# Performance work log

Measured on AMD Instinct MI355X. Metric: run time of the kernel, lower is better.

The kernel has to match this reference:

```python
import jax, jax.numpy as jnp
import numpy as np

KERNEL = 5
DILATIONS = (3, 1)
N_HEADS = 8
LN_EPS = 1e-5


def unfold1d(x, kernel, dilation, pad):
    # x: (N, H, S) -> (N, H, S, kernel) dilated sliding windows (same length)
    xp = jnp.pad(x, ((0, 0), (0, 0), (pad, pad)))
    S = x.shape[-1]
    idx = jnp.arange(S)[:, None] + jnp.arange(kernel)[None, :] * dilation  # (S, K)
    return xp[:, :, idx]  # (N, H, S, K)


def dilated_mha(q, k, v, Ws, bs, Wo, bo):
    # q,k,v: (B, S, D); Ws: (2, split, split); Wo: (D, D)
    B, S, D = q.shape
    ndil = len(DILATIONS)
    hpd = N_HEADS // ndil            # heads per dilation
    dk = D // N_HEADS
    split = D // ndil
    scale = dk ** (-0.5)
    outs, probs = [], []
    for i, dil in enumerate(DILATIONS):
        pad = dil * (KERNEL - 1) // 2
        sl = slice(i * split, (i + 1) * split)
        qi = q[..., sl] @ Ws[i].T + bs[i]
        ki = k[..., sl] @ Ws[i].T + bs[i]
        vi = v[..., sl] @ Ws[i].T + bs[i]
        # (B,S,hpd,dk) -> (B,dk,hpd,S), matching torch transpose(1,2).permute(0,3,1,2)
        to4 = lambda x: jnp.transpose(x.reshape(B, S, hpd, dk), (0, 3, 2, 1))
        qi4, ki4, vi4 = to4(qi), to4(ki), to4(vi)
        # unfold then reinterpret (B*dk,hpd,...) as (B*hpd,dk,...) exactly as torch .reshape does
        kp = unfold1d(ki4.reshape(B * dk, hpd, S), KERNEL, dil, pad).reshape(B * hpd, dk, S, KERNEL)
        vp = unfold1d(vi4.reshape(B * dk, hpd, S), KERNEL, dil, pad).reshape(B * hpd, dk, S, KERNEL)
        qr = qi4.reshape(B * hpd, dk, S)
        scores = jnp.einsum('nds,ndsk->nsk', qr, kp) * scale   # (B*hpd, S, K)
        p = jax.nn.softmax(scores, axis=-1)
        out = jnp.einsum('nsk,ndsk->nds', p, vp)               # (B*hpd, dk, S)
        out = jnp.transpose(out.reshape(B, hpd, dk, S), (0, 3, 1, 2)).reshape(B, S, split)
        outs.append(out)
        probs.append(p.reshape(B, hpd, S, KERNEL))
    o = jnp.concatenate(outs, axis=-1) @ Wo.T + bo
    return o, jnp.concatenate(probs, axis=1)


def layer_norm(x, g, b):
    mu = jnp.mean(x, axis=-1, keepdims=True)
    var = jnp.mean((x - mu) ** 2, axis=-1, keepdims=True)
    return (x - mu) * jax.lax.rsqrt(var + LN_EPS) * g + b


def setup_inputs() -> dict:
    key = jax.random.key(0)
    ks = jax.random.split(key, 6)
    B, S, D = 32, 2048, 256
    split = D // 2
    q_emb = jax.random.normal(ks[0], (B, S, D), dtype=jnp.float32)
    s_emb = jax.random.normal(ks[1], (B, S, D), dtype=jnp.float32)
    lens = jax.random.randint(ks[2], (B,), 5, S, dtype=jnp.int32)
    W_lin = jax.random.normal(ks[3], (3, 2, split, split), dtype=jnp.float32) * (split ** -0.5)
    b_lin = jnp.zeros((3, 2, split), dtype=jnp.float32)
    W_out = jax.random.normal(ks[4], (3, D, D), dtype=jnp.float32) * (D ** -0.5)
    b_out = jnp.zeros((3, D), dtype=jnp.float32)
    ln_g = jnp.ones((3, D), dtype=jnp.float32)
    ln_b = jnp.zeros((3, D), dtype=jnp.float32)
    return {"q_emb": q_emb, "s_emb": s_emb, "lens": lens, "W_lin": W_lin,
            "b_lin": b_lin, "W_out": W_out, "b_out": b_out, "ln_g": ln_g, "ln_b": ln_b}


def reference(q_emb, s_emb, lens, W_lin, b_lin, W_out, b_out, ln_g, ln_b):
    # CASTransformer.forward, shortcut=True path, eval mode (dropout=id, mask unused)
    a1, _ = dilated_mha(q_emb, q_emb, q_emb, W_lin[0], b_lin[0], W_out[0], b_out[0])
    hq = layer_norm(q_emb + a1, ln_g[0], ln_b[0])
    a2, q_scores = dilated_mha(s_emb, s_emb, s_emb, W_lin[1], b_lin[1], W_out[1], b_out[1])
    hs = layer_norm(s_emb + a2, ln_g[1], ln_b[1])
    a3, _ = dilated_mha(hq, hq, hs, W_lin[2], b_lin[2], W_out[2], b_out[2])
    z = layer_norm(hq + a3, ln_g[2], ln_b[2])
    return z, q_scores
```

## Files before the change

kernel.cpp:

```cpp
#include <hip/hip_runtime.h>
#include <hip/hip_bf16.h>

typedef __bf16 bf16x8 __attribute__((ext_vector_type(8)));
typedef float  f32x4  __attribute__((ext_vector_type(4)));
typedef unsigned int u32;
typedef u32 u32x4 __attribute__((ext_vector_type(4)));
typedef unsigned short ushort_t;

__device__ inline float bf2f(ushort_t h) {
    union { u32 u; float f; } v; v.u = ((u32)h) << 16; return v.f;
}
__device__ inline ushort_t f2bf(float f) {
    union { float f; u32 u; } v; v.f = f;
    u32 u = v.u;
    return (ushort_t)((u + 0x7fffu + ((u >> 16) & 1u)) >> 16);
}
__device__ inline bf16x8 load_bf8(const ushort_t* p) {
    u32x4 u = *reinterpret_cast<const u32x4*>(p);
    return __builtin_bit_cast(bf16x8, u);
}
__device__ inline bf16x8 load8_in(const void* base, size_t idx, int f32flag) {
    if (!f32flag) return load_bf8((const ushort_t*)base + idx);
    const float* pf = (const float*)base + idx;
    f32x4 a = *reinterpret_cast<const f32x4*>(pf);
    f32x4 b = *reinterpret_cast<const f32x4*>(pf + 4);
    bf16x8 r;
#pragma unroll
    for (int j = 0; j < 4; ++j) { r[j] = (__bf16)a[j]; r[4 + j] = (__bf16)b[j]; }
    return r;
}
__device__ inline float ld_in(const void* base, size_t idx, int f32flag) {
    return f32flag ? ((const float*)base)[idx] : bf2f(((const ushort_t*)base)[idx]);
}

__device__ inline int pofs(int row, int ch) { return row * 256 + (ch ^ ((row & 15) << 3)); }
__device__ inline int tofs(int tr, int ch) { return tr * 256 + (ch ^ (((tr + 8) & 15) << 3)); }

__device__ inline int f_of(const int* flags, int i) { return i < 0 ? 0 : flags[i]; }
__device__ inline int out_f32(const int* flags) {
    return flags[0] | flags[1] | flags[3] | flags[4] | flags[5] | flags[6] | flags[7] | flags[8];
}

__global__ __launch_bounds__(256) void detect_all(
    const u32* a0, const u32* a1, const u32* a2, const u32* a3,
    const u32* a4, const u32* a5, const u32* a6, const u32* a7,
    int* __restrict__ flags)
{
    const u32* arrs[8] = {a0, a1, a2, a3, a4, a5, a6, a7};
    const int  ns[8]   = {16384, 16384, 16384, 384, 16384, 384, 384, 384};
    const int  fi[8]   = {0, 1, 3, 4, 5, 6, 7, 8};
    const int  b = blockIdx.x;
    const u32* d = arrs[b];
    const int  n = ns[b];

    const int t = threadIdx.x;
    int cn = 0, co = 0;
    for (int i = t; i < n; i += 256) {
        const u32 w = d[i];
        const u32 e  = (w >> 7) & 0xFF;
        const u32 fe = (w >> 23) & 0xFF;
        cn += (e >= 100 && e <= 135) ? 1 : 0;
        co += (((w & 0xFFFFu) == 0u) && fe >= 100 && fe <= 140) ? 1 : 0;
    }
    __shared__ int sn[256], so[256];
    sn[t] = cn; so[t] = co; __syncthreads();
    for (int o = 128; o; o >>= 1) {
        if (t < o) { sn[t] += sn[t + o]; so[t] += so[t + o]; }
        __syncthreads();
    }
    if (t == 0) {
        const int CN = sn[0], CO = so[0];
        const int is_f32 = (2 * CN < n) && ((2 * CO > n) || (20 * CN > n));
        flags[fi[b]] = is_f32 ? 1 : 0;
    }
}

__global__ __launch_bounds__(256, 4) void proj2_kernel(
    const void* X0, int xi0, size_t lw0, size_t lb0, ushort_t* __restrict__ Y0,
    const void* X1, int xi1, size_t lw1, size_t lb1, ushort_t* __restrict__ Y1,
    const void* __restrict__ W, const void* __restrict__ Bv, const int* __restrict__ flags)
{
    __shared__ __align__(16) ushort_t tile[64 * 256];
    const int half = blockIdx.x >> 10;
    const void* X = half ? X1 : X0;
    const int   xi = half ? xi1 : xi0;
    const size_t lw = half ? lw1 : lw0;
    const size_t lb = half ? lb1 : lb0;
    ushort_t* Y = half ? Y1 : Y0;

    const int xf  = f_of(flags, xi);
    const int wf  = flags[3], bfl = flags[4];
    const int tid = threadIdx.x;
    const int m0  = (blockIdx.x & 1023) * 64;

    if (xf) {
#pragma unroll
        for (int b = 0; b < 2; ++b) {
            f32x4 va[4], vb[4];
#pragma unroll
            for (int i = 0; i < 4; ++i) {
                const int c = tid + 256 * (4 * b + i);
                const int row = c >> 5, cc = c & 31;
                const float* pf = (const float*)X + (size_t)(m0 + row) * 256 + cc * 8;
                va[i] = *reinterpret_cast<const f32x4*>(pf);
                vb[i] = *reinterpret_cast<const f32x4*>(pf + 4);
            }
#pragma unroll
            for (int i = 0; i < 4; ++i) {
                const int c = tid + 256 * (4 * b + i);
                const int row = c >> 5, cc = c & 31;
                bf16x8 r;
#pragma unroll
                for (int j = 0; j < 4; ++j) { r[j] = (__bf16)va[i][j]; r[4 + j] = (__bf16)vb[i][j]; }
                *reinterpret_cast<u32x4*>(&tile[pofs(row, cc * 8)]) = __builtin_bit_cast(u32x4, r);
            }
        }
    } else {
        u32x4 v[8];
#pragma unroll
        for (int i = 0; i < 8; ++i) {
            const int c = tid + 256 * i;
            const int row = c >> 5, cc = c & 31;
            v[i] = *reinterpret_cast<const u32x4*>((const ushort_t*)X + (size_t)(m0 + row) * 256 + cc * 8);
        }
#pragma unroll
        for (int i = 0; i < 8; ++i) {
            const int c = tid + 256 * i;
            const int row = c >> 5, cc = c & 31;
            *reinterpret_cast<u32x4*>(&tile[pofs(row, cc * 8)]) = v[i];
        }
    }
    __syncthreads();

    const int wave = tid >> 6, lane = tid & 63;
    const int dil  = wave >> 1;
    const int n_off = (wave & 1) * 64;
    const int l15  = lane & 15, quad = lane >> 4;

    f32x4 acc[4][4] = {};
    for (int kc = 0; kc < 4; ++kc) {
        bf16x8 a[4], b[4];
#pragma unroll
        for (int mt = 0; mt < 4; ++mt)
            a[mt] = load_bf8(&tile[pofs(mt * 16 + l15, dil * 128 + kc * 32 + quad * 8)]);
#pragma unroll
        for (int nt = 0; nt < 4; ++nt)
            b[nt] = load8_in(W, lw + (size_t)dil * 16384 +
                             (size_t)(n_off + nt * 16 + l15) * 128 + kc * 32 + quad * 8, wf);
#pragma unroll
        for (int mt = 0; mt < 4; ++mt)
#pragma unroll
            for (int nt = 0; nt < 4; ++nt)
                acc[mt][nt] = __builtin_amdgcn_mfma_f32_16x16x32_bf16(a[mt], b[nt], acc[mt][nt], 0, 0, 0);
    }
    __syncthreads();

#pragma unroll
    for (int nt = 0; nt < 4; ++nt) {
        const int ncol = n_off + nt * 16 + l15;
        const float bias = ld_in(Bv, lb + dil * 128 + ncol, bfl);
#pragma unroll
        for (int mt = 0; mt < 4; ++mt)
#pragma unroll
            for (int r = 0; r < 4; ++r) {
                const int row = mt * 16 + quad * 4 + r;
                tile[pofs(row, dil * 128 + ncol)] = f2bf(acc[mt][nt][r] + bias);
            }
    }
    __syncthreads();

#pragma unroll
    for (int i = 0; i < 8; ++i) {
        const int c = tid + 256 * i;
        const int row = c >> 5, cc = c & 31;
        *reinterpret_cast<u32x4*>(Y + (size_t)(m0 + row) * 256 + cc * 8) =
            *reinterpret_cast<const u32x4*>(&tile[row * 256 + cc * 8]);
    }
}

__global__ __launch_bounds__(256, 4) void fused2_kernel(
    const ushort_t* P0, const ushort_t* V0, const void* R0, int ri0,
    size_t lw0, size_t lb0, size_t lg0, void* H0, int h0, void* pr0,
    const ushort_t* P1, const ushort_t* V1, const void* R1, int ri1,
    size_t lw1, size_t lb1, size_t lg1, void* H1, int h1, void* pr1,
    const void* __restrict__ W, const void* __restrict__ Bv,
    const void* __restrict__ G, const void* __restrict__ Bt,
    const int* __restrict__ flags)
{
    __shared__ __align__(16) ushort_t tile[80 * 256];
    float (*lsum)[64] = (float (*)[64])(&tile[0]);
    float (*lsq)[64]  = (float (*)[64])(&tile[1024]);

    const int half = blockIdx.x >> 10;
    const ushort_t* P = half ? P1 : P0;
    const ushort_t* V = half ? V1 : V0;
    const void* R  = half ? R1 : R0;
    const int   ri = half ? ri1 : ri0;
    const size_t lw = half ? lw1 : lw0;
    const size_t lb = half ? lb1 : lb0;
    const size_t lg = half ? lg1 : lg0;
    void* H        = half ? H1 : H0;
    const int h_out = half ? h1 : h0;
    void* probs_base = half ? pr1 : pr0;

    const int wf = flags[5], bvf = flags[6], gf = flags[7], btf = flags[8];
    const int rf = f_of(flags, ri);
    const int og = out_f32(flags);
    const int of = h_out ? og : 0;

    const int tid  = threadIdx.x;
    const int wave = tid >> 6, lane = tid & 63;
    const int l15  = lane & 15, quad = lane >> 4;
    const int m0   = (blockIdx.x & 1023) * 64;
    const int bb   = m0 >> 11;
    const int s0   = m0 & 2047;
    const size_t rowbase = (size_t)bb * 2048;
    const float scale = 0.17677669529663687f;

    {
        u32x4 stg[10];
#pragma unroll
        for (int i = 0; i < 10; ++i) {
            const int c = tid + 256 * i;
            const int tr = c >> 5, cc = c & 31;
            int s = s0 - 8 + tr; s = s < 0 ? 0 : (s > 2047 ? 2047 : s);
            stg[i] = *reinterpret_cast<const u32x4*>(P + (rowbase + s) * 256 + cc * 8);
        }
#pragma unroll
        for (int i = 0; i < 10; ++i) {
            const int c = tid + 256 * i;
            const int tr = c >> 5, cc = c & 31;
            *reinterpret_cast<u32x4*>(&tile[tr * 256 + cc * 8]) = stg[i];
        }
    }
    __syncthreads();

    const bool sepv = (V != P);
    u32x4 vstg[10];
    if (sepv) {
#pragma unroll
        for (int i = 0; i < 10; ++i) {
            const int c = tid + 256 * i;
            const int tr = c >> 5, cc = c & 31;
            int s2 = s0 - 8 + tr; s2 = s2 < 0 ? 0 : (s2 > 2047 ? 2047 : s2);
            vstg[i] = *reinterpret_cast<const u32x4*>(V + (rowbase + s2) * 256 + cc * 8);
        }
    }

    const int r = lane, g = wave;
    const int s = s0 + r;

    float p2[2][5];
#pragma unroll
    for (int it = 0; it < 2; ++it) {
        const int dil  = it;
        const int dila = dil ? 1 : 3;
        const int ch0  = dil * 128 + g * 8;

        float qv[4][8];
#pragma unroll
        for (int h = 0; h < 4; ++h) {
            bf16x8 t = load_bf8(&tile[tofs(8 + r, ch0 + h * 32)]);
#pragma unroll
            for (int j = 0; j < 8; ++j) qv[h][j] = (float)t[j];
        }
        float sc[5];
#pragma unroll
        for (int kk = 0; kk < 5; ++kk) {
            const int sp = s + (kk - 2) * dila;
            float a = 0.f;
            if (sp >= 0 && sp < 2048) {
                const int tr2 = 8 + r + (kk - 2) * dila;
#pragma unroll
                for (int h = 0; h < 4; ++h) {
                    bf16x8 t = load_bf8(&tile[tofs(tr2, ch0 + h * 32)]);
#pragma unroll
                    for (int j = 0; j < 8; ++j) a += qv[h][j] * (float)t[j];
                }
                a *= scale;
            }
            sc[kk] = a;
        }
        float mx = sc[0];
#pragma unroll
        for (int kk = 1; kk < 5; ++kk) mx = fmaxf(mx, sc[kk]);
        float sum = 0.f;
#pragma unroll
        for (int kk = 0; kk < 5; ++kk) { p2[it][kk] = __expf(sc[kk] - mx); sum += p2[it][kk]; }
        const float inv = 1.f / sum;
#pragma unroll
        for (int kk = 0; kk < 5; ++kk) p2[it][kk] *= inv;

        if (probs_base != nullptr) {
            const size_t pb = 16777216 + ((size_t)((bb * 8 + dil * 4 + g) * 2048 + s)) * 5;
            if (og) {
                float* pp = (float*)probs_base;
#pragma unroll
                for (int kk = 0; kk < 5; ++kk) pp[pb + kk] = p2[it][kk];
            } else {
                ushort_t* pp = (ushort_t*)probs_base;
#pragma unroll
                for (int kk = 0; kk < 5; ++kk) pp[pb + kk] = f2bf(p2[it][kk]);
            }
        }
    }

    if (sepv) {
        __syncthreads();
#pragma unroll
        for (int i = 0; i < 10; ++i) {
            const int c = tid + 256 * i;
            const int tr = c >> 5, cc = c & 31;
            *reinterpret_cast<u32x4*>(&tile[tr * 256 + cc * 8]) = vstg[i];
        }
        __syncthreads();
    }

    u32x4 wpk[2][4];
#pragma unroll
    for (int it = 0; it < 2; ++it) {
        const int dil  = it;
        const int dila = dil ? 1 : 3;
        const int ch0  = dil * 128 + g * 8;
        float o[4][8] = {};
#pragma unroll
        for (int kk = 0; kk < 5; ++kk) {
            const int sp = s + (kk - 2) * dila;
            if (sp < 0 || sp >= 2048) continue;
            const int tr2 = 8 + r + (kk - 2) * dila;
#pragma unroll
            for (int h = 0; h < 4; ++h) {
                bf16x8 t = load_bf8(&tile[tofs(tr2, ch0 + h * 32)]);
#pragma unroll
                for (int j = 0; j < 8; ++j) o[h][j] += p2[it][kk] * (float)t[j];
            }
        }
#pragma unroll
        for (int c = 0; c < 4; ++c) {
            u32x4 w;
#pragma unroll
            for (int t4 = 0; t4 < 4; ++t4) {
                const int d2a = c * 8 + t4 * 2, d2b = d2a + 1;
                const u32 lo = f2bf(o[d2a & 3][d2a >> 2]);
                const u32 hi = f2bf(o[d2b & 3][d2b >> 2]);
                w[t4] = lo | (hi << 16);
            }
            wpk[it][c] = w;
        }
    }
    __syncthreads();

#pragma unroll
    for (int it = 0; it < 2; ++it)
#pragma unroll
        for (int c = 0; c < 4; ++c)
            *reinterpret_cast<u32x4*>(&tile[tofs(8 + r, it * 128 + g * 32 + c * 8)]) = wpk[it][c];
    __syncthreads();

    const int n_off = wave * 64;

    f32x4 acc[4][4] = {};
    for (int kc = 0; kc < 8; ++kc) {
        bf16x8 a[4], b[4];
#pragma unroll
        for (int mt = 0; mt < 4; ++mt)
            a[mt] = load_bf8(&tile[tofs(8 + mt * 16 + l15, kc * 32 + quad * 8)]);
#pragma unroll
        for (int nt = 0; nt < 4; ++nt)
            b[nt] = load8_in(W, lw + (size_t)(n_off + nt * 16 + l15) * 256 + kc * 32 + quad * 8, wf);
#pragma unroll
        for (int mt = 0; mt < 4; ++mt)
#pragma unroll
            for (int nt = 0; nt < 4; ++nt)
                acc[mt][nt] = __builtin_amdgcn_mfma_f32_16x16x32_bf16(a[mt], b[nt], acc[mt][nt], 0, 0, 0);
    }

    float bias[4];
#pragma unroll
    for (int nt = 0; nt < 4; ++nt) bias[nt] = ld_in(Bv, lb + n_off + nt * 16 + l15, bvf);

    float psum[4][4] = {}, psq[4][4] = {};
#pragma unroll
    for (int mt = 0; mt < 4; ++mt) {
#pragma unroll
        for (int rr = 0; rr < 4; ++rr) {
            const size_t rrow = (size_t)(m0 + mt * 16 + quad * 4 + rr) * 256 + l15;
#pragma unroll
            for (int nt = 0; nt < 4; ++nt) {
                float v = acc[mt][nt][rr] + bias[nt] + ld_in(R, rrow + n_off + nt * 16, rf);
                acc[mt][nt][rr] = v;
                psum[mt][rr] += v;
                psq[mt][rr]  += v * v;
            }
        }
    }
#pragma unroll
    for (int off = 1; off <= 8; off <<= 1) {
#pragma unroll
        for (int mt = 0; mt < 4; ++mt)
#pragma unroll
            for (int rr = 0; rr < 4; ++rr) {
                psum[mt][rr] += __shfl_xor(psum[mt][rr], off);
                psq[mt][rr]  += __shfl_xor(psq[mt][rr],  off);
            }
    }
    if (l15 == 0) {
#pragma unroll
        for (int mt = 0; mt < 4; ++mt)
#pragma unroll
            for (int rr = 0; rr < 4; ++rr) {
                const int row = mt * 16 + quad * 4 + rr;
                lsum[wave][row] = psum[mt][rr];
                lsq[wave][row]  = psq[mt][rr];
            }
    }
    __syncthreads();

    float gl[4], blv[4];
#pragma unroll
    for (int nt = 0; nt < 4; ++nt) {
        gl[nt]  = ld_in(G,  lg + n_off + nt * 16 + l15, gf);
        blv[nt] = ld_in(Bt, lg + n_off + nt * 16 + l15, btf);
    }
#pragma unroll
    for (int mt = 0; mt < 4; ++mt) {
#pragma unroll
        for (int rr = 0; rr < 4; ++rr) {
            const int row = mt * 16 + quad * 4 + rr;
            const float sm = lsum[0][row] + lsum[1][row] + lsum[2][row] + lsum[3][row];
            const float q2 = lsq[0][row]  + lsq[1][row]  + lsq[2][row]  + lsq[3][row];
            const float mu  = sm * (1.f / 256.f);
            const float var = q2 * (1.f / 256.f) - mu * mu;
            const float rs  = rsqrtf(var + 1e-5f);
#pragma unroll
            for (int nt = 0; nt < 4; ++nt)
                acc[mt][nt][rr] = (acc[mt][nt][rr] - mu) * rs * gl[nt] + blv[nt];
        }
    }
    __syncthreads();

    if (of) {
        float* tf = (float*)tile;
#pragma unroll
        for (int hh = 0; hh < 2; ++hh) {
#pragma unroll
            for (int mh = 0; mh < 2; ++mh) {
                const int mt = 2 * hh + mh;
#pragma unroll
                for (int rr = 0; rr < 4; ++rr) {
                    const int lrow = mh * 16 + quad * 4 + rr;
#pragma unroll
                    for (int nt = 0; nt < 4; ++nt)
                        tf[lrow * 256 + n_off + nt * 16 + l15] = acc[mt][nt][rr];
                }
            }
            __syncthreads();
#pragma unroll
            for (int i = 0; i < 8; ++i) {
                const int c = tid + 256 * i;
                const int row = c >> 6, cc = c & 63;
                *reinterpret_cast<f32x4*>((float*)H + (size_t)(m0 + hh * 32 + row) * 256 + cc * 4) =
                    *reinterpret_cast<const f32x4*>(&tf[row * 256 + cc * 4]);
            }
            __syncthreads();
        }
    } else {
#pragma unroll
        for (int mt = 0; mt < 4; ++mt)
#pragma unroll
            for (int rr = 0; rr < 4; ++rr) {
                const int row = mt * 16 + quad * 4 + rr;
#pragma unroll
                for (int nt = 0; nt < 4; ++nt)
                    tile[pofs(row, n_off + nt * 16 + l15)] = f2bf(acc[mt][nt][rr]);
            }
        __syncthreads();
#pragma unroll
        for (int i = 0; i < 8; ++i) {
            const int c = tid + 256 * i;
            const int row = c >> 5, cc = c & 31;
            const int sc8 = (cc * 8) ^ ((row & 15) << 3);
            *reinterpret_cast<u32x4*>((ushort_t*)H + (size_t)(m0 + row) * 256 + cc * 8) =
                *reinterpret_cast<const u32x4*>(&tile[row * 256 + sc8]);
        }
    }
}

extern "C" void kernel_launch(void* const* d_in, const int* in_sizes, int n_in,
                              void* d_out, int out_size, void* d_ws, size_t ws_size,
                              hipStream_t stream) {
    const void* q_emb = d_in[0];
    const void* s_emb = d_in[1];
    const void* W_lin = d_in[3];
    const void* b_lin = d_in[4];
    const void* W_out = d_in[5];
    const void* b_out = d_in[6];
    const void* ln_g  = d_in[7];
    const void* ln_b  = d_in[8];

    const size_t SLOT = 16777216;
    int*      flags = (int*)d_ws;
    ushort_t* S1 = (ushort_t*)((char*)d_ws + 256);
    ushort_t* S2 = S1 + SLOT;
    ushort_t* S3 = S1 + 2 * SLOT;
    ushort_t* S4 = S1 + 3 * SLOT;
    const size_t need4 = 256 + 4 * SLOT * sizeof(ushort_t);

    const dim3 blk(256);
    detect_all<<<8, blk, 0, stream>>>((const u32*)q_emb, (const u32*)s_emb, (const u32*)W_lin,
        (const u32*)b_lin, (const u32*)W_out, (const u32*)b_out,
        (const u32*)ln_g, (const u32*)ln_b, flags);

    proj2_kernel<<<2048, blk, 0, stream>>>(q_emb, 0, 0, 0, S1,
                                           s_emb, 1, 32768, 256, S2,
                                           W_lin, b_lin, flags);

    if (ws_size >= need4) {
        fused2_kernel<<<2048, blk, 0, stream>>>(
            S1, S1, q_emb, 0, 0,     0,   0,   S3, 0, nullptr,
            S2, S2, s_emb, 1, 65536, 256, 256, S4, 0, d_out,
            W_out, b_out, ln_g, ln_b, flags);
        proj2_kernel<<<2048, blk, 0, stream>>>(S3, -1, 65536, 512, S1,
                                               S4, -1, 65536, 512, S2,
                                               W_lin, b_lin, flags);
        fused2_kernel<<<1024, blk, 0, stream>>>(
            S1, S2, S3, -1, 131072, 512, 512, d_out, 1, nullptr,
            S1, S2, S3, -1, 131072, 512, 512, d_out, 1, nullptr,
            W_out, b_out, ln_g, ln_b, flags);
    } else {
        fused2_kernel<<<1024, blk, 0, stream>>>(
            S1, S1, q_emb, 0, 0, 0, 0, S3, 0, nullptr,
            S1, S1, q_emb, 0, 0, 0, 0, S3, 0, nullptr,
            W_out, b_out, ln_g, ln_b, flags);
        fused2_kernel<<<1024, blk, 0, stream>>>(
            S2, S2, s_emb, 1, 65536, 256, 256, S1, 0, d_out,
            S2, S2, s_emb, 1, 65536, 256, 256, S1, 0, d_out,
            W_out, b_out, ln_g, ln_b, flags);
        proj2_kernel<<<2048, blk, 0, stream>>>(S3, -1, 65536, 512, S2,
                                               S1, -1, 65536, 512, S1,
                                               W_lin, b_lin, flags);
        fused2_kernel<<<1024, blk, 0, stream>>>(
            S2, S1, S3, -1, 131072, 512, 512, d_out, 1, nullptr,
            S2, S1, S3, -1, 131072, 512, 512, d_out, 1, nullptr,
            W_out, b_out, ln_g, ln_b, flags);
    }
}
```

Baseline: 562.1 us.

## Software-pipeline proj2 over four 32-row tiles with double-buffered LDS

Each proj2 block now handles four consecutive 32-row tiles instead of one 64-row tile, so the grid halves to 1024 blocks. The next tile's input is loaded into registers while the current tile's MFMA runs, then stored into a second LDS buffer, which hides global load latency. LDS per block stays at 32KB. The trade-off is fewer blocks, smaller M per MFMA pass (W fragments are reloaded per tile, so W reuse per load halves), and extra registers for the prefetch. A compiler memory barrier is also added in fused2.

```diff
diff --git a/kernel.cpp b/kernel.cpp
--- a/kernel.cpp
+++ b/kernel.cpp
@@ -80,8 +80,8 @@
     const void* X1, int xi1, size_t lw1, size_t lb1, ushort_t* __restrict__ Y1,
     const void* __restrict__ W, const void* __restrict__ Bv, const int* __restrict__ flags)
 {
-    __shared__ __align__(16) ushort_t tile[64 * 256];
-    const int half = blockIdx.x >> 10;
+    __shared__ __align__(16) ushort_t buf[2][32 * 256];
+    const int half = blockIdx.x >> 9;
     const void* X = half ? X1 : X0;
     const int   xi = half ? xi1 : xi0;
     const size_t lw = half ? lw1 : lw0;
@@ -91,90 +91,86 @@
     const int xf  = f_of(flags, xi);
     const int wf  = flags[3], bfl = flags[4];
     const int tid = threadIdx.x;
-    const int m0  = (blockIdx.x & 1023) * 64;
-
-    if (xf) {
-#pragma unroll
-        for (int b = 0; b < 2; ++b) {
-            f32x4 va[4], vb[4];
-#pragma unroll
-            for (int i = 0; i < 4; ++i) {
-                const int c = tid + 256 * (4 * b + i);
-                const int row = c >> 5, cc = c & 31;
-                const float* pf = (const float*)X + (size_t)(m0 + row) * 256 + cc * 8;
-                va[i] = *reinterpret_cast<const f32x4*>(pf);
-                vb[i] = *reinterpret_cast<const f32x4*>(pf + 4);
-            }
-#pragma unroll
-            for (int i = 0; i < 4; ++i) {
-                const int c = tid + 256 * (4 * b + i);
-                const int row = c >> 5, cc = c & 31;
-                bf16x8 r;
-#pragma unroll
-                for (int j = 0; j < 4; ++j) { r[j] = (__bf16)va[i][j]; r[4 + j] = (__bf16)vb[i][j]; }
-                *reinterpret_cast<u32x4*>(&tile[pofs(row, cc * 8)]) = __builtin_bit_cast(u32x4, r);
-            }
-        }
-    } else {
-        u32x4 v[8];
-#pragma unroll
-        for (int i = 0; i < 8; ++i) {
-            const int c = tid + 256 * i;
-            const int row = c >> 5, cc = c & 31;
-            v[i] = *reinterpret_cast<const u32x4*>((const ushort_t*)X + (size_t)(m0 + row) * 256 + cc * 8);
-        }
-#pragma unroll
-        for (int i = 0; i < 8; ++i) {
-            const int c = tid + 256 * i;
-            const int row = c >> 5, cc = c & 31;
-            *reinterpret_cast<u32x4*>(&tile[pofs(row, cc * 8)]) = v[i];
-        }
-    }
-    __syncthreads();
+    const int base = (blockIdx.x & 511) * 4;
 
     const int wave = tid >> 6, lane = tid & 63;
     const int dil  = wave >> 1;
     const int n_off = (wave & 1) * 64;
     const int l15  = lane & 15, quad = lane >> 4;
 
-    f32x4 acc[4][4] = {};
-    for (int kc = 0; kc < 4; ++kc) {
-        bf16x8 a[4], b[4];
-#pragma unroll
-        for (int mt = 0; mt < 4; ++mt)
-            a[mt] = load_bf8(&tile[pofs(mt * 16 + l15, dil * 128 + kc * 32 + quad * 8)]);
-#pragma unroll
-        for (int nt = 0; nt < 4; ++nt)
-            b[nt] = load8_in(W, lw + (size_t)dil * 16384 +
-                             (size_t)(n_off + nt * 16 + l15) * 128 + kc * 32 + quad * 8, wf);
-#pragma unroll
-        for (int mt = 0; mt < 4; ++mt)
-#pragma unroll
-            for (int nt = 0; nt < 4; ++nt)
-                acc[mt][nt] = __builtin_amdgcn_mfma_f32_16x16x32_bf16(a[mt], b[nt], acc[mt][nt], 0, 0, 0);
-    }
-    __syncthreads();
-
-#pragma unroll
-    for (int nt = 0; nt < 4; ++nt) {
-        const int ncol = n_off + nt * 16 + l15;
-        const float bias = ld_in(Bv, lb + dil * 128 + ncol, bfl);
-#pragma unroll
-        for (int mt = 0; mt < 4; ++mt)
-#pragma unroll
-            for (int r = 0; r < 4; ++r) {
-                const int row = mt * 16 + quad * 4 + r;
-                tile[pofs(row, dil * 128 + ncol)] = f2bf(acc[mt][nt][r] + bias);
-            }
-    }
-    __syncthreads();
-
-#pragma unroll
-    for (int i = 0; i < 8; ++i) {
+#pragma unroll
+    for (int i = 0; i < 4; ++i) {
         const int c = tid + 256 * i;
         const int row = c >> 5, cc = c & 31;
-        *reinterpret_cast<u32x4*>(Y + (size_t)(m0 + row) * 256 + cc * 8) =
-            *reinterpret_cast<const u32x4*>(&tile[row * 256 + cc * 8]);
+        bf16x8 v = load8_in(X, (size_t)(base * 32 + row) * 256 + cc * 8, xf);
+        *reinterpret_cast<u32x4*>(&buf[0][pofs(row, cc * 8)]) = __builtin_bit_cast(u32x4, v);
+    }
+    __syncthreads();
+
+    for (int t = 0; t < 4; ++t) {
+        const int cur = t & 1, nxt = cur ^ 1;
+        const int m0 = (base + t) * 32;
+
+        bf16x8 rc[4];
+        if (t < 3) {
+            const int m1 = (base + t + 1) * 32;
+#pragma unroll
+            for (int i = 0; i < 4; ++i) {
+                const int c = tid + 256 * i;
+                const int row = c >> 5, cc = c & 31;
+                rc[i] = load8_in(X, (size_t)(m1 + row) * 256 + cc * 8, xf);
+            }
+        }
+        asm volatile("" ::: "memory");
+
+        f32x4 acc[2][4] = {};
+        for (int kc = 0; kc < 4; ++kc) {
+            bf16x8 a[2], b[4];
+#pragma unroll
+            for (int mt = 0; mt < 2; ++mt)
+                a[mt] = load_bf8(&buf[cur][pofs(mt * 16 + l15, dil * 128 + kc * 32 + quad * 8)]);
+#pragma unroll
+            for (int nt = 0; nt < 4; ++nt)
+                b[nt] = load8_in(W, lw + (size_t)dil * 16384 +
+                                 (size_t)(n_off + nt * 16 + l15) * 128 + kc * 32 + quad * 8, wf);
+#pragma unroll
+            for (int mt = 0; mt < 2; ++mt)
+#pragma unroll
+                for (int nt = 0; nt < 4; ++nt)
+                    acc[mt][nt] = __builtin_amdgcn_mfma_f32_16x16x32_bf16(a[mt], b[nt], acc[mt][nt], 0, 0, 0);
+        }
+        __syncthreads();
+
+#pragma unroll
+        for (int nt = 0; nt < 4; ++nt) {
+            const int ncol = n_off + nt * 16 + l15;
+            const float bias = ld_in(Bv, lb + dil * 128 + ncol, bfl);
+#pragma unroll
+            for (int mt = 0; mt < 2; ++mt)
+#pragma unroll
+                for (int r = 0; r < 4; ++r) {
+                    const int row = mt * 16 + quad * 4 + r;
+                    buf[cur][pofs(row, dil * 128 + ncol)] = f2bf(acc[mt][nt][r] + bias);
+                }
+        }
+        if (t < 3) {
+#pragma unroll
+            for (int i = 0; i < 4; ++i) {
+                const int c = tid + 256 * i;
+                const int row = c >> 5, cc = c & 31;
+                *reinterpret_cast<u32x4*>(&buf[nxt][pofs(row, cc * 8)]) =
+                    __builtin_bit_cast(u32x4, rc[i]);
+            }
+        }
+        __syncthreads();
+
+#pragma unroll
+        for (int i = 0; i < 4; ++i) {
+            const int c = tid + 256 * i;
+            const int row = c >> 5, cc = c & 31;
+            *reinterpret_cast<u32x4*>(Y + (size_t)(m0 + row) * 256 + cc * 8) =
+                *reinterpret_cast<const u32x4*>(&buf[cur][row * 256 + cc * 8]);
+        }
     }
 }
 
@@ -246,6 +242,7 @@
             vstg[i] = *reinterpret_cast<const u32x4*>(V + (rowbase + s2) * 256 + cc * 8);
         }
     }
+    asm volatile("" ::: "memory");
 
     const int r = lane, g = wave;
     const int s = s0 + r;
@@ -511,7 +508,7 @@
         (const u32*)b_lin, (const u32*)W_out, (const u32*)b_out,
         (const u32*)ln_g, (const u32*)ln_b, flags);
 
-    proj2_kernel<<<2048, blk, 0, stream>>>(q_emb, 0, 0, 0, S1,
+    proj2_kernel<<<1024, blk, 0, stream>>>(q_emb, 0, 0, 0, S1,
                                            s_emb, 1, 32768, 256, S2,
                                            W_lin, b_lin, flags);
 
@@ -520,7 +517,7 @@
             S1, S1, q_emb, 0, 0,     0,   0,   S3, 0, nullptr,
             S2, S2, s_emb, 1, 65536, 256, 256, S4, 0, d_out,
             W_out, b_out, ln_g, ln_b, flags);
-        proj2_kernel<<<2048, blk, 0, stream>>>(S3, -1, 65536, 512, S1,
+        proj2_kernel<<<1024, blk, 0, stream>>>(S3, -1, 65536, 512, S1,
                                                S4, -1, 65536, 512, S2,
                                                W_lin, b_lin, flags);
         fused2_kernel<<<1024, blk, 0, stream>>>(
@@ -536,7 +533,7 @@
             S2, S2, s_emb, 1, 65536, 256, 256, S1, 0, d_out,
             S2, S2, s_emb, 1, 65536, 256, 256, S1, 0, d_out,
             W_out, b_out, ln_g, ln_b, flags);
-        proj2_kernel<<<2048, blk, 0, stream>>>(S3, -1, 65536, 512, S2,
+        proj2_kernel<<<1024, blk, 0, stream>>>(S3, -1, 65536, 512, S2,
                                                S1, -1, 65536, 512, S1,
                                                W_lin, b_lin, flags);
         fused2_kernel<<<1024, blk, 0, stream>>>(
```

New measurement: 695.1 us. 1.24x slower.
